# Optimization experiments

Hardware: AMD Instinct MI355X
Metric: run time of the kernel (lower is better)

Reference implementation:

```python
import jax, jax.numpy as jnp
import numpy as np

NUM_P = 8192   # number of forward particles
M = 8192       # number of backward smoothing samples
DX = 16        # state dim
DU = 8         # action dim
SIGMA = 1.0    # transition noise std (Gaussian env)


def setup_inputs() -> dict:
    key = jax.random.key(0)
    ks = jax.random.split(key, 7)
    particles = jax.random.normal(ks[0], (NUM_P, DX + DU), dtype=jnp.float32)
    log_weights = jax.random.normal(ks[1], (NUM_P,), dtype=jnp.float32)
    samples_p = jax.random.normal(ks[2], (M, DX), dtype=jnp.float32)
    weights = jax.random.normal(ks[3], (M,), dtype=jnp.float32)
    A = jax.random.normal(ks[4], (DX, DX), dtype=jnp.float32) * 0.1
    B = jax.random.normal(ks[5], (DX, DU), dtype=jnp.float32) * 0.1
    samples_idx = jax.random.randint(ks[6], (NUM_P,), 0, NUM_P)
    return {"particles": particles, "log_weights": log_weights,
            "samples_p": samples_p, "weights": weights,
            "A": A, "B": B, "samples_idx": samples_idx}


def reference(particles, log_weights, samples_p, weights, A, B, samples_idx):
    # backward_smoothing (Doucet et al.): for each backward sample p,
    #   forward_ll = env.log_likelihood(x, u, p)  over all particles
    #   lls = forward_ll - logsumexp(log_weights + forward_ll) + weight
    #   smoothed = logsumexp over samples; log_weights += smoothed
    dx = A.shape[0]
    x = particles[:, :dx]            # [P, DX]
    u = particles[:, dx:]            # [P, DU]
    mu = x @ A.T + u @ B.T           # predicted next state, [P, DX]
    # squared distance via gram trick -> only [M, P] materialized
    sq = (jnp.sum(samples_p * samples_p, axis=1)[:, None]
          + jnp.sum(mu * mu, axis=1)[None, :]
          - 2.0 * samples_p @ mu.T)                      # [M, P]
    log_const = 0.5 * dx * jnp.log(2.0 * jnp.pi * SIGMA * SIGMA)
    forward_ll = -0.5 * sq / (SIGMA * SIGMA) - log_const  # [M, P]
    # per-sample normalization
    norm = jax.scipy.special.logsumexp(log_weights[None, :] + forward_ll, axis=1)  # [M]
    lls = forward_ll - norm[:, None] + weights[:, None]   # [M, P]
    smoothed = jax.scipy.special.logsumexp(lls, axis=0)   # [P]
    new_log_weights = log_weights + smoothed
    return new_log_weights
```

## Files before the change

### kernel.cpp

```cpp
#include <hip/hip_runtime.h>
#include <string.h>

#define LOG2E 1.44269504088896340736f
#define LN2   0.69314718055994530942f

typedef _Float16 f16x8 __attribute__((ext_vector_type(8)));
typedef __attribute__((ext_vector_type(2))) float f32x2;
typedef __attribute__((ext_vector_type(4))) float f32x4;
typedef __attribute__((ext_vector_type(16))) float f32x16;

#define WS_MUP  0
#define WS_SPT  65536
#define WS_AV1  131072
#define WS_P1   139264
#define WS_P2   663552

__device__ __forceinline__ float fast_exp2(float x) {
#if __has_builtin(__builtin_amdgcn_exp2f)
  return __builtin_amdgcn_exp2f(x);
#else
  return exp2f(x);
#endif
}
__device__ __forceinline__ float fast_log2(float x) {
#if __has_builtin(__builtin_amdgcn_logf)
  return __builtin_amdgcn_logf(x);
#else
  return log2f(x);
#endif
}

__device__ __forceinline__ void pack_row_f16(const float* v, unsigned int* buf) {
#pragma unroll
  for (int k = 0; k < 16; k += 2) {
    _Float16 h0 = (_Float16)v[k];
    _Float16 h1 = (_Float16)v[k + 1];
    unsigned short u0, u1;
    memcpy(&u0, &h0, 2);
    memcpy(&u1, &h1, 2);
    buf[k >> 1] = (unsigned int)u0 | ((unsigned int)u1 << 16);
  }
}

__global__ __launch_bounds__(256) void k_prep(
    const float* __restrict__ particles, const float* __restrict__ lw,
    const float* __restrict__ sp,
    const float* __restrict__ A, const float* __restrict__ B,
    unsigned int* __restrict__ muP, unsigned int* __restrict__ spT,
    float* __restrict__ av1) {
  int j = blockIdx.x * 256 + threadIdx.x;
  float x[24];
  {
    const float4* p4 = (const float4*)(particles + (size_t)j * 24);
#pragma unroll
    for (int q = 0; q < 6; ++q) {
      float4 v = p4[q];
      x[q * 4 + 0] = v.x; x[q * 4 + 1] = v.y; x[q * 4 + 2] = v.z; x[q * 4 + 3] = v.w;
    }
  }
  float mrow[16];
  float m2 = 0.f;
#pragma unroll
  for (int k = 0; k < 16; ++k) {
    float s = 0.f;
#pragma unroll
    for (int l = 0; l < 16; ++l) s += x[l] * A[k * 16 + l];
#pragma unroll
    for (int l = 0; l < 8; ++l) s += x[16 + l] * B[k * 8 + l];
    mrow[k] = s;
    m2 += s * s;
  }
  av1[j] = LOG2E * (lw[j] - 0.5f * m2);

  unsigned int buf[8];
  pack_row_f16(mrow, buf);
  {
    uint4* dst = (uint4*)(muP + (size_t)j * 8);
    dst[0] = make_uint4(buf[0], buf[1], buf[2], buf[3]);
    dst[1] = make_uint4(buf[4], buf[5], buf[6], buf[7]);
  }
  float srow[16];
  {
    const float4* s4 = (const float4*)(sp + (size_t)j * 16);
#pragma unroll
    for (int q = 0; q < 4; ++q) {
      float4 v = s4[q];
      srow[q * 4 + 0] = LOG2E * v.x; srow[q * 4 + 1] = LOG2E * v.y;
      srow[q * 4 + 2] = LOG2E * v.z; srow[q * 4 + 3] = LOG2E * v.w;
    }
  }
  pack_row_f16(srow, buf);
  {
    uint4* dst = (uint4*)(spT + (size_t)j * 8);
    dst[0] = make_uint4(buf[0], buf[1], buf[2], buf[3]);
    dst[1] = make_uint4(buf[4], buf[5], buf[6], buf[7]);
  }
}

#define EXPSUM16(d, acc2)                                             \
  {                                                                   \
    f32x2 p0, p1, p2, p3, p4, p5, p6, p7;                             \
    p0[0] = fast_exp2(d[0]);  p0[1] = fast_exp2(d[1]);                \
    p1[0] = fast_exp2(d[2]);  p1[1] = fast_exp2(d[3]);                \
    p2[0] = fast_exp2(d[4]);  p2[1] = fast_exp2(d[5]);                \
    p3[0] = fast_exp2(d[6]);  p3[1] = fast_exp2(d[7]);                \
    p4[0] = fast_exp2(d[8]);  p4[1] = fast_exp2(d[9]);                \
    p5[0] = fast_exp2(d[10]); p5[1] = fast_exp2(d[11]);               \
    p6[0] = fast_exp2(d[12]); p6[1] = fast_exp2(d[13]);               \
    p7[0] = fast_exp2(d[14]); p7[1] = fast_exp2(d[15]);               \
    f32x2 s0 = p0 + p1, s1 = p2 + p3, s2 = p4 + p5, s3 = p6 + p7;     \
    acc2 += (s0 + s1) + (s2 + s3);                                    \
  }

__global__ __launch_bounds__(256, 4) void k_pass(
    const unsigned int* __restrict__ tilev,
    const unsigned int* __restrict__ statv,
    const float* __restrict__ avv,
    const float* __restrict__ psrc,
    float* __restrict__ part) {
  __shared__ __align__(16) unsigned int tl[128 * 12];
  __shared__ __align__(64) float av_l[128];
  __shared__ float sums[256];
  __shared__ float av_raw[128];
  const int t = threadIdx.x;
  const int chunk = blockIdx.x;
  const int sg    = blockIdx.y;

  {
    const uint4* src = (const uint4*)(tilev + (size_t)chunk * 1024);
    int row = t >> 1, s = t & 1;
    *(uint4*)(tl + row * 12 + s * 4) = src[t];
  }

  if (psrc == nullptr) {
    if (t < 128) {
      int src = (t & 96) + ((t >> 2) & 3) * 8 + ((t >> 4) & 1) * 4 + (t & 3);
      av_l[t] = avv[chunk * 128 + src];
    }
  } else {
    const int row = t & 127, half = t >> 7;
    float s = 0.f;
    const float* p = psrc + (size_t)(half * 32) * 8192 + chunk * 128 + row;
#pragma unroll 8
    for (int c = 0; c < 32; ++c) s += p[(size_t)c * 8192];
    sums[t] = s;
    __syncthreads();
    if (t < 128)
      av_raw[t] = LOG2E * avv[chunk * 128 + t] - fast_log2(sums[t] + sums[t + 128]);
    __syncthreads();
    if (t < 128) {
      int src = (t & 96) + ((t >> 2) & 3) * 8 + ((t >> 4) & 1) * 4 + (t & 3);
      av_l[t] = av_raw[src];
    }
  }
  __syncthreads();

  const int l = t & 63;
  const int wave = t >> 6;
  const int lr = l & 31;
  const int hi = l >> 5;
  const int r0 = sg * 512 + wave * 128;

  const f16x8 b0 = *(const f16x8*)(statv + (size_t)(r0 + lr) * 8 + hi * 4);
  const f16x8 b1 = *(const f16x8*)(statv + (size_t)(r0 + 32 + lr) * 8 + hi * 4);
  const f16x8 b2 = *(const f16x8*)(statv + (size_t)(r0 + 64 + lr) * 8 + hi * 4);
  const f16x8 b3 = *(const f16x8*)(statv + (size_t)(r0 + 96 + lr) * 8 + hi * 4);

  f32x2 acc2_0 = {0.f, 0.f}, acc2_1 = {0.f, 0.f};
  f32x2 acc2_2 = {0.f, 0.f}, acc2_3 = {0.f, 0.f};
#pragma unroll
  for (int tile = 0; tile < 4; ++tile) {
    const f16x8 a = *(const f16x8*)(tl + (tile * 32 + lr) * 12 + hi * 4);
    const f32x16 C = *(const f32x16*)(av_l + tile * 32 + hi * 16);

    {
      f32x16 d0 = __builtin_amdgcn_mfma_f32_32x32x16_f16(a, b0, C, 0, 0, 0);
      f32x16 d1 = __builtin_amdgcn_mfma_f32_32x32x16_f16(a, b1, C, 0, 0, 0);
      EXPSUM16(d0, acc2_0)
      EXPSUM16(d1, acc2_1)
    }
    {
      f32x16 d2 = __builtin_amdgcn_mfma_f32_32x32x16_f16(a, b2, C, 0, 0, 0);
      f32x16 d3 = __builtin_amdgcn_mfma_f32_32x32x16_f16(a, b3, C, 0, 0, 0);
      EXPSUM16(d2, acc2_2)
      EXPSUM16(d3, acc2_3)
    }
  }
  float acc0 = acc2_0[0] + acc2_0[1];
  float acc1 = acc2_1[0] + acc2_1[1];
  float acc2 = acc2_2[0] + acc2_2[1];
  float acc3 = acc2_3[0] + acc2_3[1];
  acc0 += __shfl_xor(acc0, 32);
  acc1 += __shfl_xor(acc1, 32);
  acc2 += __shfl_xor(acc2, 32);
  acc3 += __shfl_xor(acc3, 32);
  float* base = part + (size_t)chunk * 8192 + r0 + lr;
  if (l < 32) { base[0]  = acc0; base[64] = acc2; }
  else        { base[32] = acc1; base[96] = acc3; }
}

__global__ __launch_bounds__(256) void k_out(
    const float* __restrict__ part, const float* __restrict__ av1,
    float* __restrict__ out) {
  int j = blockIdx.x * 256 + threadIdx.x;
  float s = 0.f;
#pragma unroll
  for (int c = 0; c < 64; ++c) s += part[(size_t)c * 8192 + j];
  out[j] = LN2 * (av1[j] + fast_log2(s));
}

extern "C" void kernel_launch(void* const* d_in, const int* in_sizes, int n_in,
                              void* d_out, int out_size, void* d_ws, size_t ws_size,
                              hipStream_t stream) {
  const float* particles = (const float*)d_in[0];
  const float* lw        = (const float*)d_in[1];
  const float* sp        = (const float*)d_in[2];
  const float* w         = (const float*)d_in[3];
  const float* A         = (const float*)d_in[4];
  const float* B         = (const float*)d_in[5];

  float* ws = (float*)d_ws;
  unsigned int* muP = (unsigned int*)(ws + WS_MUP);
  unsigned int* spT = (unsigned int*)(ws + WS_SPT);
  float* av1  = ws + WS_AV1;
  float* p1   = ws + WS_P1;
  float* p2   = ws + WS_P2;
  float* out  = (float*)d_out;

  k_prep<<<dim3(32), dim3(256), 0, stream>>>(particles, lw, sp, A, B, muP, spT, av1);
  k_pass<<<dim3(64, 16), dim3(256), 0, stream>>>(muP, spT, av1, nullptr, p1);
  k_pass<<<dim3(64, 16), dim3(256), 0, stream>>>(spT, muP, w, p1, p2);
  k_out<<<dim3(32), dim3(256), 0, stream>>>(p2, av1, out);
}
```

Measured before the change: 44.02 us.

## Fuse prep kernel into first pass, recomputing mu and fp16 conversion per block

Removes the separate k_prep launch. Pass 1 now computes mu = xA^T + uB^T and the av1 terms for its 128-particle chunk directly, and converts samples_p to fp16 on the fly. Pass 2 converts its own sample tile from fp32. This saves one launch and a round trip through workspace, but each of the 16 sg blocks redundantly recomputes the chunk's mu and reads fp32 sample data instead of packed fp16.

Result: faster. 42.07 us, median of 2 (-4.4%).

```diff
diff --git a/kernel.cpp b/kernel.cpp
--- a/kernel.cpp
+++ b/kernel.cpp
@@ -6,14 +6,12 @@
 
 typedef _Float16 f16x8 __attribute__((ext_vector_type(8)));
 typedef __attribute__((ext_vector_type(2))) float f32x2;
-typedef __attribute__((ext_vector_type(4))) float f32x4;
 typedef __attribute__((ext_vector_type(16))) float f32x16;
 
 #define WS_MUP  0
-#define WS_SPT  65536
-#define WS_AV1  131072
-#define WS_P1   139264
-#define WS_P2   663552
+#define WS_AV1  65536
+#define WS_P1   73728
+#define WS_P2   598016
 
 __device__ __forceinline__ float fast_exp2(float x) {
 #if __has_builtin(__builtin_amdgcn_exp2f)
@@ -30,71 +28,17 @@
 #endif
 }
 
-__device__ __forceinline__ void pack_row_f16(const float* v, unsigned int* buf) {
-#pragma unroll
-  for (int k = 0; k < 16; k += 2) {
-    _Float16 h0 = (_Float16)v[k];
-    _Float16 h1 = (_Float16)v[k + 1];
-    unsigned short u0, u1;
-    memcpy(&u0, &h0, 2);
-    memcpy(&u1, &h1, 2);
-    buf[k >> 1] = (unsigned int)u0 | ((unsigned int)u1 << 16);
-  }
-}
-
-__global__ __launch_bounds__(256) void k_prep(
-    const float* __restrict__ particles, const float* __restrict__ lw,
-    const float* __restrict__ sp,
-    const float* __restrict__ A, const float* __restrict__ B,
-    unsigned int* __restrict__ muP, unsigned int* __restrict__ spT,
-    float* __restrict__ av1) {
-  int j = blockIdx.x * 256 + threadIdx.x;
-  float x[24];
-  {
-    const float4* p4 = (const float4*)(particles + (size_t)j * 24);
-#pragma unroll
-    for (int q = 0; q < 6; ++q) {
-      float4 v = p4[q];
-      x[q * 4 + 0] = v.x; x[q * 4 + 1] = v.y; x[q * 4 + 2] = v.z; x[q * 4 + 3] = v.w;
-    }
-  }
-  float mrow[16];
-  float m2 = 0.f;
-#pragma unroll
-  for (int k = 0; k < 16; ++k) {
-    float s = 0.f;
-#pragma unroll
-    for (int l = 0; l < 16; ++l) s += x[l] * A[k * 16 + l];
-#pragma unroll
-    for (int l = 0; l < 8; ++l) s += x[16 + l] * B[k * 8 + l];
-    mrow[k] = s;
-    m2 += s * s;
-  }
-  av1[j] = LOG2E * (lw[j] - 0.5f * m2);
-
-  unsigned int buf[8];
-  pack_row_f16(mrow, buf);
-  {
-    uint4* dst = (uint4*)(muP + (size_t)j * 8);
-    dst[0] = make_uint4(buf[0], buf[1], buf[2], buf[3]);
-    dst[1] = make_uint4(buf[4], buf[5], buf[6], buf[7]);
-  }
-  float srow[16];
-  {
-    const float4* s4 = (const float4*)(sp + (size_t)j * 16);
-#pragma unroll
-    for (int q = 0; q < 4; ++q) {
-      float4 v = s4[q];
-      srow[q * 4 + 0] = LOG2E * v.x; srow[q * 4 + 1] = LOG2E * v.y;
-      srow[q * 4 + 2] = LOG2E * v.z; srow[q * 4 + 3] = LOG2E * v.w;
-    }
-  }
-  pack_row_f16(srow, buf);
-  {
-    uint4* dst = (uint4*)(spT + (size_t)j * 8);
-    dst[0] = make_uint4(buf[0], buf[1], buf[2], buf[3]);
-    dst[1] = make_uint4(buf[4], buf[5], buf[6], buf[7]);
-  }
+__device__ __forceinline__ unsigned int pack2_f16(float a, float b) {
+  _Float16 h0 = (_Float16)a;
+  _Float16 h1 = (_Float16)b;
+  unsigned short u0, u1;
+  memcpy(&u0, &h0, 2);
+  memcpy(&u1, &h1, 2);
+  return (unsigned int)u0 | ((unsigned int)u1 << 16);
+}
+
+__device__ __forceinline__ int av_swz(int t) {
+  return (t & 96) + ((t >> 2) & 3) * 8 + ((t >> 4) & 1) * 4 + (t & 3);
 }
 
 #define EXPSUM16(d, acc2)                                             \
@@ -112,67 +56,16 @@
     acc2 += (s0 + s1) + (s2 + s3);                                    \
   }
 
-__global__ __launch_bounds__(256, 4) void k_pass(
-    const unsigned int* __restrict__ tilev,
-    const unsigned int* __restrict__ statv,
-    const float* __restrict__ avv,
-    const float* __restrict__ psrc,
-    float* __restrict__ part) {
-  __shared__ __align__(16) unsigned int tl[128 * 12];
-  __shared__ __align__(64) float av_l[128];
-  __shared__ float sums[256];
-  __shared__ float av_raw[128];
-  const int t = threadIdx.x;
-  const int chunk = blockIdx.x;
-  const int sg    = blockIdx.y;
-
-  {
-    const uint4* src = (const uint4*)(tilev + (size_t)chunk * 1024);
-    int row = t >> 1, s = t & 1;
-    *(uint4*)(tl + row * 12 + s * 4) = src[t];
-  }
-
-  if (psrc == nullptr) {
-    if (t < 128) {
-      int src = (t & 96) + ((t >> 2) & 3) * 8 + ((t >> 4) & 1) * 4 + (t & 3);
-      av_l[t] = avv[chunk * 128 + src];
-    }
-  } else {
-    const int row = t & 127, half = t >> 7;
-    float s = 0.f;
-    const float* p = psrc + (size_t)(half * 32) * 8192 + chunk * 128 + row;
-#pragma unroll 8
-    for (int c = 0; c < 32; ++c) s += p[(size_t)c * 8192];
-    sums[t] = s;
-    __syncthreads();
-    if (t < 128)
-      av_raw[t] = LOG2E * avv[chunk * 128 + t] - fast_log2(sums[t] + sums[t + 128]);
-    __syncthreads();
-    if (t < 128) {
-      int src = (t & 96) + ((t >> 2) & 3) * 8 + ((t >> 4) & 1) * 4 + (t & 3);
-      av_l[t] = av_raw[src];
-    }
-  }
-  __syncthreads();
-
-  const int l = t & 63;
-  const int wave = t >> 6;
-  const int lr = l & 31;
-  const int hi = l >> 5;
-  const int r0 = sg * 512 + wave * 128;
-
-  const f16x8 b0 = *(const f16x8*)(statv + (size_t)(r0 + lr) * 8 + hi * 4);
-  const f16x8 b1 = *(const f16x8*)(statv + (size_t)(r0 + 32 + lr) * 8 + hi * 4);
-  const f16x8 b2 = *(const f16x8*)(statv + (size_t)(r0 + 64 + lr) * 8 + hi * 4);
-  const f16x8 b3 = *(const f16x8*)(statv + (size_t)(r0 + 96 + lr) * 8 + hi * 4);
-
+__device__ __forceinline__ void inner_core(
+    const f16x8 b0, const f16x8 b1, const f16x8 b2, const f16x8 b3,
+    const unsigned int* __restrict__ tl, const float* __restrict__ av_l,
+    float* __restrict__ part, int chunk, int r0, int lr, int hi, int l) {
   f32x2 acc2_0 = {0.f, 0.f}, acc2_1 = {0.f, 0.f};
   f32x2 acc2_2 = {0.f, 0.f}, acc2_3 = {0.f, 0.f};
 #pragma unroll
   for (int tile = 0; tile < 4; ++tile) {
     const f16x8 a = *(const f16x8*)(tl + (tile * 32 + lr) * 12 + hi * 4);
     const f32x16 C = *(const f32x16*)(av_l + tile * 32 + hi * 16);
-
     {
       f32x16 d0 = __builtin_amdgcn_mfma_f32_32x32x16_f16(a, b0, C, 0, 0, 0);
       f32x16 d1 = __builtin_amdgcn_mfma_f32_32x32x16_f16(a, b1, C, 0, 0, 0);
@@ -199,6 +92,135 @@
   else        { base[32] = acc1; base[96] = acc3; }
 }
 
+__global__ __launch_bounds__(256, 4) void k_pass1(
+    const float* __restrict__ particles, const float* __restrict__ lw,
+    const float* __restrict__ sp,
+    const float* __restrict__ A, const float* __restrict__ B,
+    unsigned int* __restrict__ muP, float* __restrict__ av1,
+    float* __restrict__ part) {
+  __shared__ __align__(16) unsigned int tl[128 * 12];
+  __shared__ __align__(64) float av_l[128];
+  __shared__ float av_raw[128];
+  const int t = threadIdx.x;
+  const int chunk = blockIdx.x;
+  const int sg    = blockIdx.y;
+
+  if (t < 128) {
+    const int j = chunk * 128 + t;
+    float x[24];
+    {
+      const float4* p4 = (const float4*)(particles + (size_t)j * 24);
+#pragma unroll
+      for (int q = 0; q < 6; ++q) {
+        float4 v = p4[q];
+        x[q * 4 + 0] = v.x; x[q * 4 + 1] = v.y; x[q * 4 + 2] = v.z; x[q * 4 + 3] = v.w;
+      }
+    }
+    float mrow[16];
+    float m2 = 0.f;
+#pragma unroll
+    for (int k = 0; k < 16; ++k) {
+      float s = 0.f;
+#pragma unroll
+      for (int l2 = 0; l2 < 16; ++l2) s += x[l2] * A[k * 16 + l2];
+#pragma unroll
+      for (int l2 = 0; l2 < 8; ++l2) s += x[16 + l2] * B[k * 8 + l2];
+      mrow[k] = s;
+      m2 += s * s;
+    }
+    unsigned int buf[8];
+#pragma unroll
+    for (int k = 0; k < 16; k += 2) buf[k >> 1] = pack2_f16(mrow[k], mrow[k + 1]);
+    *(uint4*)(tl + t * 12 + 0) = make_uint4(buf[0], buf[1], buf[2], buf[3]);
+    *(uint4*)(tl + t * 12 + 4) = make_uint4(buf[4], buf[5], buf[6], buf[7]);
+    float av = LOG2E * (lw[j] - 0.5f * m2);
+    av_raw[t] = av;
+    if (sg == 0) {
+      uint4* dst = (uint4*)(muP + (size_t)j * 8);
+      dst[0] = make_uint4(buf[0], buf[1], buf[2], buf[3]);
+      dst[1] = make_uint4(buf[4], buf[5], buf[6], buf[7]);
+      av1[j] = av;
+    }
+  }
+  __syncthreads();
+  if (t < 128) av_l[t] = av_raw[av_swz(t)];
+  __syncthreads();
+
+  const int l = t & 63;
+  const int wave = t >> 6;
+  const int lr = l & 31;
+  const int hi = l >> 5;
+  const int r0 = sg * 512 + wave * 128;
+
+  f16x8 b[4];
+#pragma unroll
+  for (int s = 0; s < 4; ++s) {
+    const float4* p4 = (const float4*)(sp + (size_t)(r0 + s * 32 + lr) * 16 + hi * 8);
+    float4 f0 = p4[0], f1 = p4[1];
+    b[s][0] = (_Float16)(LOG2E * f0.x); b[s][1] = (_Float16)(LOG2E * f0.y);
+    b[s][2] = (_Float16)(LOG2E * f0.z); b[s][3] = (_Float16)(LOG2E * f0.w);
+    b[s][4] = (_Float16)(LOG2E * f1.x); b[s][5] = (_Float16)(LOG2E * f1.y);
+    b[s][6] = (_Float16)(LOG2E * f1.z); b[s][7] = (_Float16)(LOG2E * f1.w);
+  }
+
+  inner_core(b[0], b[1], b[2], b[3], tl, av_l, part, chunk, r0, lr, hi, l);
+}
+
+__global__ __launch_bounds__(256, 4) void k_pass2(
+    const float* __restrict__ sp,
+    const unsigned int* __restrict__ statv,
+    const float* __restrict__ w,
+    const float* __restrict__ psrc,
+    float* __restrict__ part) {
+  __shared__ __align__(16) unsigned int tl[128 * 12];
+  __shared__ __align__(64) float av_l[128];
+  __shared__ float sums[256];
+  __shared__ float av_raw[128];
+  const int t = threadIdx.x;
+  const int chunk = blockIdx.x;
+  const int sg    = blockIdx.y;
+
+  {
+    const int row = t >> 1, h2 = t & 1;
+    const float4* p4 = (const float4*)(sp + (size_t)(chunk * 128 + row) * 16 + h2 * 8);
+    float4 f0 = p4[0], f1 = p4[1];
+    unsigned int buf[4];
+    buf[0] = pack2_f16(LOG2E * f0.x, LOG2E * f0.y);
+    buf[1] = pack2_f16(LOG2E * f0.z, LOG2E * f0.w);
+    buf[2] = pack2_f16(LOG2E * f1.x, LOG2E * f1.y);
+    buf[3] = pack2_f16(LOG2E * f1.z, LOG2E * f1.w);
+    *(uint4*)(tl + row * 12 + h2 * 4) = make_uint4(buf[0], buf[1], buf[2], buf[3]);
+  }
+
+  {
+    const int row = t & 127, half = t >> 7;
+    float s = 0.f;
+    const float* p = psrc + (size_t)(half * 32) * 8192 + chunk * 128 + row;
+#pragma unroll 8
+    for (int c = 0; c < 32; ++c) s += p[(size_t)c * 8192];
+    sums[t] = s;
+    __syncthreads();
+    if (t < 128)
+      av_raw[t] = LOG2E * w[chunk * 128 + t] - fast_log2(sums[t] + sums[t + 128]);
+    __syncthreads();
+    if (t < 128) av_l[t] = av_raw[av_swz(t)];
+  }
+  __syncthreads();
+
+  const int l = t & 63;
+  const int wave = t >> 6;
+  const int lr = l & 31;
+  const int hi = l >> 5;
+  const int r0 = sg * 512 + wave * 128;
+
+  const f16x8 b0 = *(const f16x8*)(statv + (size_t)(r0 + lr) * 8 + hi * 4);
+  const f16x8 b1 = *(const f16x8*)(statv + (size_t)(r0 + 32 + lr) * 8 + hi * 4);
+  const f16x8 b2 = *(const f16x8*)(statv + (size_t)(r0 + 64 + lr) * 8 + hi * 4);
+  const f16x8 b3 = *(const f16x8*)(statv + (size_t)(r0 + 96 + lr) * 8 + hi * 4);
+
+  inner_core(b0, b1, b2, b3, tl, av_l, part, chunk, r0, lr, hi, l);
+}
+
 __global__ __launch_bounds__(256) void k_out(
     const float* __restrict__ part, const float* __restrict__ av1,
     float* __restrict__ out) {
@@ -221,14 +243,12 @@
 
   float* ws = (float*)d_ws;
   unsigned int* muP = (unsigned int*)(ws + WS_MUP);
-  unsigned int* spT = (unsigned int*)(ws + WS_SPT);
   float* av1  = ws + WS_AV1;
   float* p1   = ws + WS_P1;
   float* p2   = ws + WS_P2;
   float* out  = (float*)d_out;
 
-  k_prep<<<dim3(32), dim3(256), 0, stream>>>(particles, lw, sp, A, B, muP, spT, av1);
-  k_pass<<<dim3(64, 16), dim3(256), 0, stream>>>(muP, spT, av1, nullptr, p1);
-  k_pass<<<dim3(64, 16), dim3(256), 0, stream>>>(spT, muP, w, p1, p2);
+  k_pass1<<<dim3(64, 16), dim3(256), 0, stream>>>(particles, lw, sp, A, B, muP, av1, p1);
+  k_pass2<<<dim3(64, 16), dim3(256), 0, stream>>>(sp, muP, w, p1, p2);
   k_out<<<dim3(32), dim3(256), 0, stream>>>(p2, av1, out);
 }
```
